# Kernel tuning notes

Hardware: AMD Instinct MI355X
Metric: run time of the kernel (lower is better)

## Reference

```python
import jax, jax.numpy as jnp
import numpy as np

N_NODES = 100000
N_EDGES = 1600000
IN_DIM = 32
OUT_DIM = 64


def setup_inputs() -> dict:
    key = jax.random.key(0)
    k1, k2, k3, k4, k5 = jax.random.split(key, 5)
    feature = jax.random.normal(k1, (N_NODES, IN_DIM), dtype=jnp.float32)
    src = jax.random.randint(k2, (N_EDGES,), 0, N_NODES, dtype=jnp.int32)
    dst = jax.random.randint(k3, (N_EDGES,), 0, N_NODES, dtype=jnp.int32)
    W = jax.random.normal(k4, (IN_DIM, OUT_DIM), dtype=jnp.float32) * (1.0 / np.sqrt(IN_DIM))
    b = jax.random.normal(k5, (OUT_DIM,), dtype=jnp.float32) * 0.01
    return {"feature": feature, "src": src, "dst": dst, "W": W, "b": b}


def reference(feature, src, dst, W, b):
    # copy_u + sum: gather source features along edges, segment-sum into dst nodes
    msgs = feature[src]  # [E, in_dim]
    h_neigh = jax.ops.segment_sum(msgs, dst, num_segments=N_NODES)  # [N, in_dim]
    # linear projection
    return h_neigh @ W + b  # [N, out_dim]
```

## Files before the change

kernel.cpp:

```cpp
#include <hip/hip_runtime.h>

#define IN_DIM 32
#define OUT_DIM 64

__global__ __launch_bounds__(256) void mpnn_scatter_kernel(
    const float* __restrict__ feature,
    const int* __restrict__ src,
    const int* __restrict__ dst,
    float* __restrict__ h,
    int n_edges) {
    long long tid = (long long)blockIdx.x * blockDim.x + threadIdx.x;
    long long total = (long long)n_edges * IN_DIM;
    if (tid >= total) return;
    int e = (int)(tid >> 5);
    int d = (int)(tid & 31);
    int s = src[e];
    int t = dst[e];
    float v = feature[(long long)s * IN_DIM + d];
    atomicAdd(&h[(long long)t * IN_DIM + d], v);
}

__global__ __launch_bounds__(256) void mpnn_proj_kernel(
    const float* __restrict__ h,
    const float* __restrict__ W,
    const float* __restrict__ b,
    float* __restrict__ out,
    int n_nodes) {
    __shared__ float Ws[IN_DIM * OUT_DIM];
    __shared__ float hs[4][IN_DIM];
    int tx = threadIdx.x;

    for (int i = tx; i < IN_DIM * OUT_DIM; i += 256) Ws[i] = W[i];

    int row0 = blockIdx.x * 4;
    if (tx < 4 * IN_DIM) {
        int r = tx >> 5, k = tx & 31;
        int row = row0 + r;
        hs[r][k] = (row < n_nodes) ? h[(long long)row * IN_DIM + k] : 0.0f;
    }
    __syncthreads();

    int col = tx & 63;
    int r = tx >> 6;
    int row = row0 + r;
    if (row >= n_nodes) return;

    float acc = b[col];
#pragma unroll
    for (int k = 0; k < IN_DIM; ++k)
        acc += hs[r][k] * Ws[k * OUT_DIM + col];

    out[(long long)row * OUT_DIM + col] = acc;
}

extern "C" void kernel_launch(void* const* d_in, const int* in_sizes, int n_in,
                              void* d_out, int out_size, void* d_ws, size_t ws_size,
                              hipStream_t stream) {
    const float* feature = (const float*)d_in[0];
    const int* src = (const int*)d_in[1];
    const int* dst = (const int*)d_in[2];
    const float* W = (const float*)d_in[3];
    const float* b = (const float*)d_in[4];
    float* out = (float*)d_out;

    int n_nodes = in_sizes[0] / IN_DIM;
    int n_edges = in_sizes[1];

    float* h = (float*)d_ws;

    hipMemsetAsync(h, 0, (size_t)n_nodes * IN_DIM * sizeof(float), stream);

    long long total = (long long)n_edges * IN_DIM;
    int threads = 256;
    int blocks = (int)((total + threads - 1) / threads);
    mpnn_scatter_kernel<<<blocks, threads, 0, stream>>>(feature, src, dst, h, n_edges);

    int pblocks = (n_nodes + 3) / 4;
    mpnn_proj_kernel<<<pblocks, 256, 0, stream>>>(h, W, b, out, n_nodes);
}
```

Measured before the change: 276.7 us.

## Bin edges into destination buckets and fuse gather, LDS reduce, and projection

Replaces the per-element global float atomics with two passes. The first pass bins each edge into a fixed-capacity bucket of 128 destination nodes, storing the source id and local destination packed into one word. The second pass gives each bucket one block, which accumulates source features in shared memory with LDS atomics and then applies the linear projection directly. This removes the global h buffer, its memset and most global atomic traffic. In exchange it has heavy contention on the few bucket cursors, and edges beyond the fixed bucket capacity are silently dropped, so it relies on a roughly uniform dst distribution.

```diff
diff --git a/kernel.cpp b/kernel.cpp
--- a/kernel.cpp
+++ b/kernel.cpp
@@ -3,54 +3,90 @@
 #define IN_DIM 32
 #define OUT_DIM 64
 
-__global__ __launch_bounds__(256) void mpnn_scatter_kernel(
-    const float* __restrict__ feature,
+#define BUCKET_SHIFT 7
+#define BUCKET_NODES (1 << BUCKET_SHIFT)
+#define CAP 2688
+#define CURSOR_STRIDE 16
+
+__global__ __launch_bounds__(256) void bucket_scatter(
     const int* __restrict__ src,
     const int* __restrict__ dst,
-    float* __restrict__ h,
+    int* __restrict__ cursors,
+    unsigned int* __restrict__ bdata,
     int n_edges) {
-    long long tid = (long long)blockIdx.x * blockDim.x + threadIdx.x;
-    long long total = (long long)n_edges * IN_DIM;
-    if (tid >= total) return;
-    int e = (int)(tid >> 5);
-    int d = (int)(tid & 31);
+    int e = blockIdx.x * 256 + threadIdx.x;
+    if (e >= n_edges) return;
     int s = src[e];
     int t = dst[e];
-    float v = feature[(long long)s * IN_DIM + d];
-    atomicAdd(&h[(long long)t * IN_DIM + d], v);
+    int b = t >> BUCKET_SHIFT;
+    int pos = atomicAdd(&cursors[b * CURSOR_STRIDE], 1);
+    if (pos < CAP) {
+        bdata[(long long)b * CAP + pos] =
+            ((unsigned int)s << BUCKET_SHIFT) | (unsigned int)(t & (BUCKET_NODES - 1));
+    }
 }
 
-__global__ __launch_bounds__(256) void mpnn_proj_kernel(
-    const float* __restrict__ h,
+__global__ __launch_bounds__(256) void bucket_gather_project(
+    const float* __restrict__ feature,
+    const unsigned int* __restrict__ bdata,
+    const int* __restrict__ cursors,
     const float* __restrict__ W,
-    const float* __restrict__ b,
+    const float* __restrict__ bias_v,
     float* __restrict__ out,
     int n_nodes) {
+    __shared__ float tile[BUCKET_NODES][IN_DIM];
     __shared__ float Ws[IN_DIM * OUT_DIM];
-    __shared__ float hs[4][IN_DIM];
     int tx = threadIdx.x;
+    int bk = blockIdx.x;
 
-    for (int i = tx; i < IN_DIM * OUT_DIM; i += 256) Ws[i] = W[i];
+    for (int i = tx; i < BUCKET_NODES * IN_DIM; i += 256)
+        (&tile[0][0])[i] = 0.0f;
+    for (int i = tx; i < IN_DIM * OUT_DIM; i += 256)
+        Ws[i] = W[i];
+    __syncthreads();
 
-    int row0 = blockIdx.x * 4;
-    if (tx < 4 * IN_DIM) {
-        int r = tx >> 5, k = tx & 31;
-        int row = row0 + r;
-        hs[r][k] = (row < n_nodes) ? h[(long long)row * IN_DIM + k] : 0.0f;
+    int cnt = cursors[bk * CURSOR_STRIDE];
+    if (cnt > CAP) cnt = CAP;
+    const unsigned int* bd = bdata + (long long)bk * CAP;
+
+    int g = tx >> 5;
+    int d = tx & 31;
+
+    int e = g;
+    for (; e + 24 < cnt; e += 32) {
+        unsigned int p0 = bd[e];
+        unsigned int p1 = bd[e + 8];
+        unsigned int p2 = bd[e + 16];
+        unsigned int p3 = bd[e + 24];
+        float v0 = feature[(long long)(p0 >> BUCKET_SHIFT) * IN_DIM + d];
+        float v1 = feature[(long long)(p1 >> BUCKET_SHIFT) * IN_DIM + d];
+        float v2 = feature[(long long)(p2 >> BUCKET_SHIFT) * IN_DIM + d];
+        float v3 = feature[(long long)(p3 >> BUCKET_SHIFT) * IN_DIM + d];
+        atomicAdd(&tile[p0 & (BUCKET_NODES - 1)][d], v0);
+        atomicAdd(&tile[p1 & (BUCKET_NODES - 1)][d], v1);
+        atomicAdd(&tile[p2 & (BUCKET_NODES - 1)][d], v2);
+        atomicAdd(&tile[p3 & (BUCKET_NODES - 1)][d], v3);
+    }
+    for (; e < cnt; e += 8) {
+        unsigned int p = bd[e];
+        float v = feature[(long long)(p >> BUCKET_SHIFT) * IN_DIM + d];
+        atomicAdd(&tile[p & (BUCKET_NODES - 1)][d], v);
     }
     __syncthreads();
 
     int col = tx & 63;
-    int r = tx >> 6;
-    int row = row0 + r;
-    if (row >= n_nodes) return;
-
-    float acc = b[col];
+    int r0 = tx >> 6;
+    int node_base = bk << BUCKET_SHIFT;
+    float acc_bias = bias_v[col];
+    for (int r = r0; r < BUCKET_NODES; r += 4) {
+        int node = node_base + r;
+        if (node >= n_nodes) break;
+        float acc = acc_bias;
 #pragma unroll
-    for (int k = 0; k < IN_DIM; ++k)
-        acc += hs[r][k] * Ws[k * OUT_DIM + col];
-
-    out[(long long)row * OUT_DIM + col] = acc;
+        for (int k = 0; k < IN_DIM; ++k)
+            acc += tile[r][k] * Ws[k * OUT_DIM + col];
+        out[(long long)node * OUT_DIM + col] = acc;
+    }
 }
 
 extern "C" void kernel_launch(void* const* d_in, const int* in_sizes, int n_in,
@@ -65,16 +101,17 @@
 
     int n_nodes = in_sizes[0] / IN_DIM;
     int n_edges = in_sizes[1];
+    int n_buckets = (n_nodes + BUCKET_NODES - 1) >> BUCKET_SHIFT;
 
-    float* h = (float*)d_ws;
+    int* cursors = (int*)d_ws;
+    unsigned int* bdata =
+        (unsigned int*)((char*)d_ws + (size_t)n_buckets * CURSOR_STRIDE * sizeof(int));
 
-    hipMemsetAsync(h, 0, (size_t)n_nodes * IN_DIM * sizeof(float), stream);
+    hipMemsetAsync(cursors, 0, (size_t)n_buckets * CURSOR_STRIDE * sizeof(int), stream);
 
-    long long total = (long long)n_edges * IN_DIM;
-    int threads = 256;
-    int blocks = (int)((total + threads - 1) / threads);
-    mpnn_scatter_kernel<<<blocks, threads, 0, stream>>>(feature, src, dst, h, n_edges);
+    int blocks = (n_edges + 255) / 256;
+    bucket_scatter<<<blocks, 256, 0, stream>>>(src, dst, cursors, bdata, n_edges);
 
-    int pblocks = (n_nodes + 3) / 4;
-    mpnn_proj_kernel<<<pblocks, 256, 0, stream>>>(h, W, b, out, n_nodes);
+    bucket_gather_project<<<n_buckets, 256, 0, stream>>>(feature, bdata, cursors, W, b, out,
+                                                         n_nodes);
 }
```

Measured after the change: 533.0 us. 92.6% more time.

## Build CSR by destination and fuse atomic-free gather-sum with projection

Applied to the files above, without the earlier changes.

Replaces per-element float atomic scatter (51M atomics) with a CSR build: a histogram of dst, a three-stage prefix scan, and a scatter of src ids into buckets. A fused kernel then gathers and sums neighbour features per node in registers and applies the linear projection from shared memory, so the intermediate h buffer is never written. This removes the float atomics and the h memset and readback, but adds several small launches plus 1.6M integer atomics. It also relies on a fixed workspace pad and on the scan2 kernel handling at most 128 scan blocks.

```diff
diff --git a/kernel.cpp b/kernel.cpp
--- a/kernel.cpp
+++ b/kernel.cpp
@@ -2,55 +2,128 @@
 
 #define IN_DIM 32
 #define OUT_DIM 64
+#define N_PAD 100352
 
-__global__ __launch_bounds__(256) void mpnn_scatter_kernel(
-    const float* __restrict__ feature,
-    const int* __restrict__ src,
-    const int* __restrict__ dst,
-    float* __restrict__ h,
-    int n_edges) {
-    long long tid = (long long)blockIdx.x * blockDim.x + threadIdx.x;
-    long long total = (long long)n_edges * IN_DIM;
-    if (tid >= total) return;
-    int e = (int)(tid >> 5);
-    int d = (int)(tid & 31);
-    int s = src[e];
-    int t = dst[e];
-    float v = feature[(long long)s * IN_DIM + d];
-    atomicAdd(&h[(long long)t * IN_DIM + d], v);
+
+__global__ __launch_bounds__(256) void csr_hist(
+    const int* __restrict__ dst, int* __restrict__ counts, int n_edges) {
+    int e = blockIdx.x * 256 + threadIdx.x;
+    if (e < n_edges) atomicAdd(&counts[dst[e]], 1);
 }
 
-__global__ __launch_bounds__(256) void mpnn_proj_kernel(
-    const float* __restrict__ h,
+__global__ __launch_bounds__(256) void csr_scan1(
+    const int* __restrict__ counts, int* __restrict__ offs,
+    int* __restrict__ bsum, int n) {
+    __shared__ int lsum[256];
+    int t = threadIdx.x;
+    int base = blockIdx.x * 1024 + t * 4;
+    int c0 = (base + 0 < n) ? counts[base + 0] : 0;
+    int c1 = (base + 1 < n) ? counts[base + 1] : 0;
+    int c2 = (base + 2 < n) ? counts[base + 2] : 0;
+    int c3 = (base + 3 < n) ? counts[base + 3] : 0;
+    int s = c0 + c1 + c2 + c3;
+    lsum[t] = s;
+    __syncthreads();
+    for (int off = 1; off < 256; off <<= 1) {
+        int v = (t >= off) ? lsum[t - off] : 0;
+        __syncthreads();
+        lsum[t] += v;
+        __syncthreads();
+    }
+    int run = lsum[t] - s;
+    if (base + 0 < n) offs[base + 0] = run;
+    run += c0;
+    if (base + 1 < n) offs[base + 1] = run;
+    run += c1;
+    if (base + 2 < n) offs[base + 2] = run;
+    run += c2;
+    if (base + 3 < n) offs[base + 3] = run;
+    if (t == 255) bsum[blockIdx.x] = lsum[255];
+}
+
+__global__ __launch_bounds__(128) void csr_scan2(
+    const int* __restrict__ bsum, int* __restrict__ top, int nb) {
+    __shared__ int ls[128];
+    int t = threadIdx.x;
+    int v0 = (t < nb) ? bsum[t] : 0;
+    ls[t] = v0;
+    __syncthreads();
+    for (int off = 1; off < 128; off <<= 1) {
+        int v = (t >= off) ? ls[t - off] : 0;
+        __syncthreads();
+        ls[t] += v;
+        __syncthreads();
+    }
+    if (t < nb) top[t] = ls[t] - v0;
+}
+
+__global__ __launch_bounds__(256) void csr_scan3(
+    int* __restrict__ offs, int* __restrict__ cursor,
+    const int* __restrict__ top, int n) {
+    int i = blockIdx.x * 256 + threadIdx.x;
+    if (i < n) {
+        int o = offs[i] + top[i >> 10];
+        offs[i] = o;
+        cursor[i] = o;
+    }
+}
+
+__global__ __launch_bounds__(256) void csr_scatter(
+    const int* __restrict__ src, const int* __restrict__ dst,
+    int* __restrict__ cursor, int* __restrict__ bdata, int n_edges) {
+    int e = blockIdx.x * 256 + threadIdx.x;
+    if (e >= n_edges) return;
+    int s = src[e];
+    int pos = atomicAdd(&cursor[dst[e]], 1);
+    bdata[pos] = s;
+}
+
+__global__ __launch_bounds__(1024) void csr_gather_proj(
+    const float* __restrict__ feature,
+    const int* __restrict__ offs,
+    const int* __restrict__ cursor,
+    const int* __restrict__ bdata,
     const float* __restrict__ W,
-    const float* __restrict__ b,
+    const float* __restrict__ bias_v,
     float* __restrict__ out,
     int n_nodes) {
     __shared__ float Ws[IN_DIM * OUT_DIM];
-    __shared__ float hs[4][IN_DIM];
+    __shared__ float hs[32][IN_DIM];
     int tx = threadIdx.x;
+    for (int i = tx; i < IN_DIM * OUT_DIM; i += 1024) Ws[i] = W[i];
 
-    for (int i = tx; i < IN_DIM * OUT_DIM; i += 256) Ws[i] = W[i];
+    int g = tx >> 5;
+    int d = tx & 31;
+    int node = blockIdx.x * 32 + g;
 
-    int row0 = blockIdx.x * 4;
-    if (tx < 4 * IN_DIM) {
-        int r = tx >> 5, k = tx & 31;
-        int row = row0 + r;
-        hs[r][k] = (row < n_nodes) ? h[(long long)row * IN_DIM + k] : 0.0f;
+    float acc = 0.0f;
+    if (node < n_nodes) {
+        int j = offs[node];
+        int end = cursor[node];
+        for (; j + 1 < end; j += 2) {
+            int sa = bdata[j];
+            int sb = bdata[j + 1];
+            acc += feature[sa * IN_DIM + d];
+            acc += feature[sb * IN_DIM + d];
+        }
+        if (j < end) acc += feature[bdata[j] * IN_DIM + d];
     }
+    hs[g][d] = acc;
     __syncthreads();
 
     int col = tx & 63;
-    int r = tx >> 6;
-    int row = row0 + r;
-    if (row >= n_nodes) return;
-
-    float acc = b[col];
+    int r0 = tx >> 6;
+    float bb = bias_v[col];
+    for (int r = r0; r < 32; r += 16) {
+        int n2 = blockIdx.x * 32 + r;
+        if (n2 < n_nodes) {
+            float a = bb;
 #pragma unroll
-    for (int k = 0; k < IN_DIM; ++k)
-        acc += hs[r][k] * Ws[k * OUT_DIM + col];
-
-    out[(long long)row * OUT_DIM + col] = acc;
+            for (int k = 0; k < IN_DIM; ++k)
+                a += hs[r][k] * Ws[k * OUT_DIM + col];
+            out[n2 * OUT_DIM + col] = a;
+        }
+    }
 }
 
 extern "C" void kernel_launch(void* const* d_in, const int* in_sizes, int n_in,
@@ -66,15 +139,26 @@
     int n_nodes = in_sizes[0] / IN_DIM;
     int n_edges = in_sizes[1];
 
-    float* h = (float*)d_ws;
+    int* counts = (int*)d_ws;
+    int* offs = counts + N_PAD;
+    int* cursor = offs + N_PAD;
+    int* bsum = cursor + N_PAD;
+    int* top = bsum + 128;
+    int* bdata = top + 128;
 
-    hipMemsetAsync(h, 0, (size_t)n_nodes * IN_DIM * sizeof(float), stream);
+    hipMemsetAsync(counts, 0, (size_t)n_nodes * sizeof(int), stream);
 
-    long long total = (long long)n_edges * IN_DIM;
-    int threads = 256;
-    int blocks = (int)((total + threads - 1) / threads);
-    mpnn_scatter_kernel<<<blocks, threads, 0, stream>>>(feature, src, dst, h, n_edges);
+    int eblocks = (n_edges + 255) / 256;
+    csr_hist<<<eblocks, 256, 0, stream>>>(dst, counts, n_edges);
 
-    int pblocks = (n_nodes + 3) / 4;
-    mpnn_proj_kernel<<<pblocks, 256, 0, stream>>>(h, W, b, out, n_nodes);
+    int sblocks = (n_nodes + 1023) / 1024;
+    csr_scan1<<<sblocks, 256, 0, stream>>>(counts, offs, bsum, n_nodes);
+    csr_scan2<<<1, 128, 0, stream>>>(bsum, top, sblocks);
+    csr_scan3<<<(n_nodes + 255) / 256, 256, 0, stream>>>(offs, cursor, top, n_nodes);
+
+    csr_scatter<<<eblocks, 256, 0, stream>>>(src, dst, cursor, bdata, n_edges);
+
+    int gblocks = (n_nodes + 31) / 32;
+    csr_gather_proj<<<gblocks, 1024, 0, stream>>>(feature, offs, cursor, bdata, W, b, out,
+                                                  n_nodes);
 }
```

Result: slower. 353.4 us (+27.7%).
